# Kernel tuning notes

Measured on AMD Instinct MI355X. Metric: run time of the kernel, lower is better.

Reference implementation:

```python
import jax, jax.numpy as jnp
import numpy as np

B, T, E, H = 32, 577, 1024, 16
D = E // H  # head_dim = 64

def setup_inputs() -> dict:
    key = jax.random.key(0)
    ks = jax.random.split(key, 5)
    s = 1.0 / np.sqrt(E)
    return {
        "x": jax.random.normal(ks[0], (B, T, E), dtype=jnp.float32),
        "Wq": jax.random.normal(ks[1], (E, E), dtype=jnp.float32) * s,
        "bq": jnp.zeros((E,), dtype=jnp.float32),
        "Wk": jax.random.normal(ks[2], (E, E), dtype=jnp.float32) * s,
        "bk": jnp.zeros((E,), dtype=jnp.float32),
        "Wv": jax.random.normal(ks[3], (E, E), dtype=jnp.float32) * s,
        "bv": jnp.zeros((E,), dtype=jnp.float32),
        "Wo": jax.random.normal(ks[4], (E, E), dtype=jnp.float32) * s,
        "bo": jnp.zeros((E,), dtype=jnp.float32),
    }

def reference(x, Wq, bq, Wk, bk, Wv, bv, Wo, bo):
    # Linear projections (torch Linear: x @ W.T + b; here W stored as [in,out])
    q = (x @ Wq + bq).reshape(B, T, H, D).transpose(0, 2, 1, 3)  # [B,H,T,D]
    k = (x @ Wk + bk).reshape(B, T, H, D).transpose(0, 2, 1, 3)
    v = (x @ Wv + bv).reshape(B, T, H, D).transpose(0, 2, 1, 3)
    scores = jnp.einsum('bhqd,bhkd->bhqk', q, k) / jnp.sqrt(jnp.float32(D))
    att = jax.nn.softmax(scores, axis=-1)  # dropout is identity in eval
    out = jnp.einsum('bhqk,bhkd->bhqd', att, v)
    out = out.transpose(0, 2, 1, 3).reshape(B, T, E)
    return out @ Wo + bo
```

## Files before the change

kernel.cpp:

```cpp
#include <hip/hip_runtime.h>
#include <cmath>

#define BDIM 32
#define TDIM 577
#define TPAD 640
#define EDIM 1024
#define HDIM 16
#define DDIM 64
#define MDIM (BDIM * TDIM)
#define MTILES 145
#define MPAD (MTILES * 128)

typedef unsigned short u16;
typedef __bf16 bf16x8 __attribute__((ext_vector_type(8)));
typedef float f32x4 __attribute__((ext_vector_type(4)));
typedef u16 u16x8 __attribute__((ext_vector_type(8)));

__device__ __forceinline__ u16 f2bf(float f) {
    unsigned int u = __float_as_uint(f);
    u = (u + 0x7FFFu + ((u >> 16) & 1u)) >> 16;
    return (u16)u;
}

__device__ __forceinline__ void gload_lds16(const void* g, void* l) {
    __builtin_amdgcn_global_load_lds(
        (const __attribute__((address_space(1))) unsigned int*)g,
        (__attribute__((address_space(3))) unsigned int*)l, 16, 0, 0);
}

__global__ __launch_bounds__(256) void cast_x(const float* __restrict__ x,
                                              u16* __restrict__ o, int nelem)
{
    int i = (blockIdx.x * 256 + threadIdx.x) * 8;
    if (i >= nelem) return;
    float4 a = *(const float4*)(x + i);
    float4 b = *(const float4*)(x + i + 4);
    u16x8 r;
    r[0] = f2bf(a.x); r[1] = f2bf(a.y); r[2] = f2bf(a.z); r[3] = f2bf(a.w);
    r[4] = f2bf(b.x); r[5] = f2bf(b.y); r[6] = f2bf(b.z); r[7] = f2bf(b.w);
    *(u16x8*)(o + i) = r;
}

__global__ __launch_bounds__(256) void cast_wt(
    const float* __restrict__ W0, const float* __restrict__ W1,
    const float* __restrict__ W2, const float* __restrict__ W3,
    u16* __restrict__ T0, u16* __restrict__ T1,
    u16* __restrict__ T2, u16* __restrict__ T3)
{
    __shared__ float tile[32][33];
    const int z = blockIdx.z;
    const float* __restrict__ W = (z == 0) ? W0 : (z == 1) ? W1 : (z == 2) ? W2 : W3;
    u16* __restrict__ T = (z == 0) ? T0 : (z == 1) ? T1 : (z == 2) ? T2 : T3;
    const int bn = blockIdx.x * 32;
    const int bk = blockIdx.y * 32;
    const int tx = threadIdx.x & 31, ty = threadIdx.x >> 5;
#pragma unroll
    for (int p = 0; p < 4; ++p) {
        int k = bk + p * 8 + ty;
        tile[p * 8 + ty][tx] = W[(size_t)k * EDIM + bn + tx];
    }
    __syncthreads();
#pragma unroll
    for (int p = 0; p < 4; ++p) {
        int n = bn + p * 8 + ty;
        T[(size_t)n * EDIM + bk + tx] = f2bf(tile[tx][p * 8 + ty]);
    }
}

__global__ __launch_bounds__(256, 4) void gemm_bf16(
    const u16* __restrict__ A,
    const u16* __restrict__ W0, const u16* __restrict__ W1, const u16* __restrict__ W2,
    const float* __restrict__ b0, const float* __restrict__ b1, const float* __restrict__ b2,
    void* __restrict__ o0, void* __restrict__ o1, void* __restrict__ o2,
    int mode)
{
    __shared__ u16 As[128 * 64];
    __shared__ u16 Bs[128 * 64];

    const int z = blockIdx.z;
    const u16* __restrict__ Wt     = (z == 0) ? W0 : ((z == 1) ? W1 : W2);
    const float* __restrict__ bias = (z == 0) ? b0 : ((z == 1) ? b1 : b2);
    void* __restrict__ dst         = (z == 0) ? o0 : ((z == 1) ? o1 : o2);

    const int tid = threadIdx.x;
    const int wave = tid >> 6;
    const int lane = tid & 63;
    const int mlane = lane & 15;
    const int quad = lane >> 4;
    const int wm = wave >> 1;
    const int wn = wave & 1;
    const int m0 = blockIdx.y * 128;
    const int n0 = blockIdx.x * 128;

    f32x4 acc[4][4];
#pragma unroll
    for (int i = 0; i < 4; ++i)
#pragma unroll
        for (int j = 0; j < 4; ++j) acc[i][j] = (f32x4)(0.f);

    for (int k0 = 0; k0 < EDIM; k0 += 64) {
#pragma unroll
        for (int r = 0; r < 4; ++r) {
            int c = r * 256 + tid;
            int p = c >> 9, row = (c >> 2) & 127, j4 = c & 3;
            int koff = k0 + p * 32 + j4 * 8;
            gload_lds16(A + (size_t)(m0 + row) * EDIM + koff,
                        &As[(r * 256 + wave * 64) * 8]);
            gload_lds16(Wt + (size_t)(n0 + row) * EDIM + koff,
                        &Bs[(r * 256 + wave * 64) * 8]);
        }
        __syncthreads();

#pragma unroll
        for (int ks = 0; ks < 2; ++ks) {
            bf16x8 af[4], bfr[4];
#pragma unroll
            for (int t = 0; t < 4; ++t) {
                af[t]  = *(const bf16x8*)&As[ks * 4096 + (wm * 64 + t * 16 + mlane) * 32 + quad * 8];
                bfr[t] = *(const bf16x8*)&Bs[ks * 4096 + (wn * 64 + t * 16 + mlane) * 32 + quad * 8];
            }
#pragma unroll
            for (int i = 0; i < 4; ++i)
#pragma unroll
                for (int j = 0; j < 4; ++j)
                    acc[i][j] = __builtin_amdgcn_mfma_f32_16x16x32_bf16(af[i], bfr[j], acc[i][j], 0, 0, 0);
        }
        __syncthreads();
    }

#pragma unroll
    for (int j = 0; j < 4; ++j) {
        int n = n0 + wn * 64 + j * 16 + mlane;
        float bv = bias[n];
        if (mode == 1) {
            float* df = (float*)dst;
#pragma unroll
            for (int i = 0; i < 4; ++i) {
                int mb = m0 + wm * 64 + i * 16 + quad * 4;
#pragma unroll
                for (int r = 0; r < 4; ++r) {
                    int gm = mb + r;
                    if (gm < MDIM) df[(size_t)gm * EDIM + n] = acc[i][j][r] + bv;
                }
            }
        } else {
            u16* db = (u16*)dst;
            int h = n >> 6, d = n & 63;
#pragma unroll
            for (int i = 0; i < 4; ++i) {
                int mb = m0 + wm * 64 + i * 16 + quad * 4;
#pragma unroll
                for (int r = 0; r < 4; ++r) {
                    int gm = mb + r;
                    if (gm < MDIM) {
                        int b = gm / TDIM, t = gm - b * TDIM;
                        u16 val = f2bf(acc[i][j][r] + bv);
                        if (z == 2)
                            db[((size_t)(b * HDIM + h) * DDIM + d) * TPAD + t] = val;
                        else
                            db[((size_t)(b * HDIM + h) * TPAD + t) * DDIM + d] = val;
                    }
                }
            }
        }
    }
}

__global__ __launch_bounds__(256) void attn_mfma(
    const u16* __restrict__ qg, const u16* __restrict__ kg,
    const u16* __restrict__ vtg, u16* __restrict__ outg)
{
    __shared__ u16 Qs[4096];
    __shared__ u16 Ks[4096];
    __shared__ u16 Vts[4096];
    __shared__ u16 Ps[4608];

    const int tid = threadIdx.x;
    const int wave = tid >> 6;
    const int lane = tid & 63;
    const int ml = lane & 15;
    const int quad = lane >> 4;
    const int h = blockIdx.y, b = blockIdx.z;
    const int q0 = blockIdx.x * 64;
    const u16* qb = qg + ((size_t)b * HDIM + h) * TPAD * DDIM;
    const u16* kb = kg + ((size_t)b * HDIM + h) * TPAD * DDIM;
    const u16* vb = vtg + ((size_t)b * HDIM + h) * DDIM * TPAD;

#pragma unroll
    for (int r = 0; r < 2; ++r) {
        int c = r * 256 + tid;
        int row = (c >> 2) & 63, kc = c >> 8, d8 = c & 3;
        gload_lds16(qb + (size_t)(q0 + row) * DDIM + kc * 32 + d8 * 8,
                    &Qs[(r * 256 + wave * 64) * 8]);
    }
    __syncthreads();

    bf16x8 aq0 = *(const bf16x8*)&Qs[(wave * 16 + ml) * 32 + quad * 8];
    bf16x8 aq1 = *(const bf16x8*)&Qs[2048 + (wave * 16 + ml) * 32 + quad * 8];

    f32x4 oacc[4];
#pragma unroll
    for (int dt = 0; dt < 4; ++dt) oacc[dt] = (f32x4)(0.f);
    float m_i[4], l_i[4];
#pragma unroll
    for (int r = 0; r < 4; ++r) { m_i[r] = -INFINITY; l_i[r] = 0.f; }

    for (int kv0 = 0; kv0 < TDIM; kv0 += 64) {
        __syncthreads();
#pragma unroll
        for (int r = 0; r < 2; ++r) {
            int c = r * 256 + tid;
            int row = (c >> 2) & 63, kc = c >> 8, d8 = c & 3;
            gload_lds16(kb + (size_t)(kv0 + row) * DDIM + kc * 32 + d8 * 8,
                        &Ks[(r * 256 + wave * 64) * 8]);
            gload_lds16(vb + (size_t)row * TPAD + kv0 + kc * 32 + d8 * 8,
                        &Vts[(r * 256 + wave * 64) * 8]);
        }
        __syncthreads();

        f32x4 sacc[4];
#pragma unroll
        for (int jt = 0; jt < 4; ++jt) {
            bf16x8 bk0 = *(const bf16x8*)&Ks[(jt * 16 + ml) * 32 + quad * 8];
            bf16x8 bk1 = *(const bf16x8*)&Ks[2048 + (jt * 16 + ml) * 32 + quad * 8];
            f32x4 sa = (f32x4)(0.f);
            sa = __builtin_amdgcn_mfma_f32_16x16x32_bf16(aq0, bk0, sa, 0, 0, 0);
            sa = __builtin_amdgcn_mfma_f32_16x16x32_bf16(aq1, bk1, sa, 0, 0, 0);
            sacc[jt] = sa;
        }

        float p[4][4];
#pragma unroll
        for (int r = 0; r < 4; ++r) {
            float cm = -INFINITY;
#pragma unroll
            for (int jt = 0; jt < 4; ++jt) {
                bool valid = (kv0 + jt * 16 + ml) < TDIM;
                float sv = valid ? sacc[jt][r] * 0.125f : -INFINITY;
                p[jt][r] = sv;
                cm = fmaxf(cm, sv);
            }
            cm = fmaxf(cm, __shfl_xor(cm, 1, 64));
            cm = fmaxf(cm, __shfl_xor(cm, 2, 64));
            cm = fmaxf(cm, __shfl_xor(cm, 4, 64));
            cm = fmaxf(cm, __shfl_xor(cm, 8, 64));
            float mn = fmaxf(m_i[r], cm);
            float alpha = __expf(m_i[r] - mn);
            float rs = 0.f;
#pragma unroll
            for (int jt = 0; jt < 4; ++jt) {
                float e = __expf(p[jt][r] - mn);
                p[jt][r] = e;
                rs += e;
            }
            rs += __shfl_xor(rs, 1, 64);
            rs += __shfl_xor(rs, 2, 64);
            rs += __shfl_xor(rs, 4, 64);
            rs += __shfl_xor(rs, 8, 64);
            l_i[r] = l_i[r] * alpha + rs;
            m_i[r] = mn;
#pragma unroll
            for (int dt = 0; dt < 4; ++dt) oacc[dt][r] *= alpha;
        }

#pragma unroll
        for (int jt = 0; jt < 4; ++jt)
#pragma unroll
            for (int r = 0; r < 4; ++r)
                Ps[wave * 1152 + (jt >> 1) * 576 + (quad * 4 + r) * 36 + (jt & 1) * 16 + ml]
                    = f2bf(p[jt][r]);
        __syncthreads();

        bf16x8 pf0 = *(const bf16x8*)&Ps[wave * 1152 + ml * 36 + quad * 8];
        bf16x8 pf1 = *(const bf16x8*)&Ps[wave * 1152 + 576 + ml * 36 + quad * 8];

#pragma unroll
        for (int dt = 0; dt < 4; ++dt) {
            bf16x8 bv0 = *(const bf16x8*)&Vts[(dt * 16 + ml) * 32 + quad * 8];
            bf16x8 bv1 = *(const bf16x8*)&Vts[2048 + (dt * 16 + ml) * 32 + quad * 8];
            oacc[dt] = __builtin_amdgcn_mfma_f32_16x16x32_bf16(pf0, bv0, oacc[dt], 0, 0, 0);
            oacc[dt] = __builtin_amdgcn_mfma_f32_16x16x32_bf16(pf1, bv1, oacc[dt], 0, 0, 0);
        }
    }

#pragma unroll
    for (int r = 0; r < 4; ++r) {
        int t = q0 + wave * 16 + quad * 4 + r;
        if (t >= TDIM) continue;
        float inv = 1.f / l_i[r];
        size_t rowoff = ((size_t)b * TDIM + t) * EDIM + h * DDIM;
#pragma unroll
        for (int dt = 0; dt < 4; ++dt)
            outg[rowoff + dt * 16 + ml] = f2bf(oacc[dt][r] * inv);
    }
}

extern "C" void kernel_launch(void* const* d_in, const int* in_sizes, int n_in,
                              void* d_out, int out_size, void* d_ws, size_t ws_size,
                              hipStream_t stream)
{
    const float* x  = (const float*)d_in[0];
    const float* Wq = (const float*)d_in[1];
    const float* bq = (const float*)d_in[2];
    const float* Wk = (const float*)d_in[3];
    const float* bk = (const float*)d_in[4];
    const float* Wv = (const float*)d_in[5];
    const float* bv = (const float*)d_in[6];
    const float* Wo = (const float*)d_in[7];
    const float* bo = (const float*)d_in[8];
    float* out = (float*)d_out;

    const size_t hsz = (size_t)BDIM * HDIM * TPAD * DDIM;
    u16* qb  = (u16*)d_ws;
    u16* kb  = qb + hsz;
    u16* vtb = kb + hsz;
    u16* xb  = vtb + hsz;
    u16* abb = xb;
    u16* wtq = xb + (size_t)MPAD * EDIM;
    u16* wtk = wtq + (size_t)EDIM * EDIM;
    u16* wtv = wtk + (size_t)EDIM * EDIM;
    u16* wto = wtv + (size_t)EDIM * EDIM;

    cast_x<<<(MDIM * EDIM / 8 + 255) / 256, 256, 0, stream>>>(x, xb, MDIM * EDIM);
    cast_wt<<<dim3(32, 32, 4), 256, 0, stream>>>(Wq, Wk, Wv, Wo, wtq, wtk, wtv, wto);

    gemm_bf16<<<dim3(EDIM / 128, MTILES, 3), 256, 0, stream>>>(
        xb, wtq, wtk, wtv, bq, bk, bv, (void*)qb, (void*)kb, (void*)vtb, 0);

    attn_mfma<<<dim3(TPAD / 64, HDIM, BDIM), 256, 0, stream>>>(qb, kb, vtb, abb);

    gemm_bf16<<<dim3(EDIM / 128, MTILES, 1), 256, 0, stream>>>(
        abb, wto, wto, wto, bo, bo, bo, (void*)out, (void*)out, (void*)out, 1);
}
```

Measured before the change: 612.2 us.

## Loop Q/K/V projections inside one block, fold softmax scale into Q, split GEMM kernels

The QKV projection kernel now runs the three projections in sequence inside each block instead of using a z grid dimension. Consecutive passes reuse the same A tile rows, which may then hit in cache, while the launch has a third as many blocks, each doing three times the work. The 1/sqrt(D) scale is folded into the Q epilogue before bf16 rounding, and the attention kernel skips masking on full key tiles. The output projection becomes its own specialised kernel without the mode branch. Fewer blocks give less parallelism and a longer tail, and scaling Q before rounding slightly changes numerics.

```diff
diff --git a/kernel.cpp b/kernel.cpp
--- a/kernel.cpp
+++ b/kernel.cpp
@@ -67,20 +67,14 @@
     }
 }
 
-__global__ __launch_bounds__(256, 4) void gemm_bf16(
-    const u16* __restrict__ A,
-    const u16* __restrict__ W0, const u16* __restrict__ W1, const u16* __restrict__ W2,
-    const float* __restrict__ b0, const float* __restrict__ b1, const float* __restrict__ b2,
-    void* __restrict__ o0, void* __restrict__ o1, void* __restrict__ o2,
-    int mode)
+__global__ __launch_bounds__(256, 4) void gemm_qkv(
+    const u16* __restrict__ A, const u16* __restrict__ Wt,
+    const float* __restrict__ bq, const float* __restrict__ bk,
+    const float* __restrict__ bv,
+    u16* __restrict__ qo, u16* __restrict__ ko, u16* __restrict__ vto)
 {
     __shared__ u16 As[128 * 64];
     __shared__ u16 Bs[128 * 64];
-
-    const int z = blockIdx.z;
-    const u16* __restrict__ Wt     = (z == 0) ? W0 : ((z == 1) ? W1 : W2);
-    const float* __restrict__ bias = (z == 0) ? b0 : ((z == 1) ? b1 : b2);
-    void* __restrict__ dst         = (z == 0) ? o0 : ((z == 1) ? o1 : o2);
 
     const int tid = threadIdx.x;
     const int wave = tid >> 6;
@@ -92,6 +86,91 @@
     const int m0 = blockIdx.y * 128;
     const int n0 = blockIdx.x * 128;
 
+    for (int z = 0; z < 3; ++z) {
+        const u16* __restrict__ W = Wt + (size_t)z * EDIM * EDIM;
+        const float* __restrict__ bias = (z == 0) ? bq : ((z == 1) ? bk : bv);
+        u16* __restrict__ dst = (z == 0) ? qo : ((z == 1) ? ko : vto);
+
+        f32x4 acc[4][4];
+#pragma unroll
+        for (int i = 0; i < 4; ++i)
+#pragma unroll
+            for (int j = 0; j < 4; ++j) acc[i][j] = (f32x4)(0.f);
+
+        for (int k0 = 0; k0 < EDIM; k0 += 64) {
+#pragma unroll
+            for (int r = 0; r < 4; ++r) {
+                int c = r * 256 + tid;
+                int p = c >> 9, row = (c >> 2) & 127, j4 = c & 3;
+                int koff = k0 + p * 32 + j4 * 8;
+                gload_lds16(A + (size_t)(m0 + row) * EDIM + koff,
+                            &As[(r * 256 + wave * 64) * 8]);
+                gload_lds16(W + (size_t)(n0 + row) * EDIM + koff,
+                            &Bs[(r * 256 + wave * 64) * 8]);
+            }
+            __syncthreads();
+
+#pragma unroll
+            for (int ks = 0; ks < 2; ++ks) {
+                bf16x8 af[4], bfr[4];
+#pragma unroll
+                for (int t = 0; t < 4; ++t) {
+                    af[t]  = *(const bf16x8*)&As[ks * 4096 + (wm * 64 + t * 16 + mlane) * 32 + quad * 8];
+                    bfr[t] = *(const bf16x8*)&Bs[ks * 4096 + (wn * 64 + t * 16 + mlane) * 32 + quad * 8];
+                }
+#pragma unroll
+                for (int i = 0; i < 4; ++i)
+#pragma unroll
+                    for (int j = 0; j < 4; ++j)
+                        acc[i][j] = __builtin_amdgcn_mfma_f32_16x16x32_bf16(af[i], bfr[j], acc[i][j], 0, 0, 0);
+            }
+            __syncthreads();
+        }
+
+#pragma unroll
+        for (int j = 0; j < 4; ++j) {
+            int n = n0 + wn * 64 + j * 16 + mlane;
+            float bvv = bias[n];
+            int h = n >> 6, d = n & 63;
+#pragma unroll
+            for (int i = 0; i < 4; ++i) {
+                int mb = m0 + wm * 64 + i * 16 + quad * 4;
+#pragma unroll
+                for (int r = 0; r < 4; ++r) {
+                    int gm = mb + r;
+                    if (gm < MDIM) {
+                        int b = gm / TDIM, t = gm - b * TDIM;
+                        float val = acc[i][j][r] + bvv;
+                        if (z == 0) val *= 0.125f;
+                        u16 vb16 = f2bf(val);
+                        if (z == 2)
+                            dst[((size_t)(b * HDIM + h) * DDIM + d) * TPAD + t] = vb16;
+                        else
+                            dst[((size_t)(b * HDIM + h) * TPAD + t) * DDIM + d] = vb16;
+                    }
+                }
+            }
+        }
+    }
+}
+
+__global__ __launch_bounds__(256, 4) void gemm_out(
+    const u16* __restrict__ A, const u16* __restrict__ Wt,
+    const float* __restrict__ bias, float* __restrict__ dst)
+{
+    __shared__ u16 As[128 * 64];
+    __shared__ u16 Bs[128 * 64];
+
+    const int tid = threadIdx.x;
+    const int wave = tid >> 6;
+    const int lane = tid & 63;
+    const int mlane = lane & 15;
+    const int quad = lane >> 4;
+    const int wm = wave >> 1;
+    const int wn = wave & 1;
+    const int m0 = blockIdx.y * 128;
+    const int n0 = blockIdx.x * 128;
+
     f32x4 acc[4][4];
 #pragma unroll
     for (int i = 0; i < 4; ++i)
@@ -131,36 +210,14 @@
 #pragma unroll
     for (int j = 0; j < 4; ++j) {
         int n = n0 + wn * 64 + j * 16 + mlane;
-        float bv = bias[n];
-        if (mode == 1) {
-            float* df = (float*)dst;
-#pragma unroll
-            for (int i = 0; i < 4; ++i) {
-                int mb = m0 + wm * 64 + i * 16 + quad * 4;
-#pragma unroll
-                for (int r = 0; r < 4; ++r) {
-                    int gm = mb + r;
-                    if (gm < MDIM) df[(size_t)gm * EDIM + n] = acc[i][j][r] + bv;
-                }
-            }
-        } else {
-            u16* db = (u16*)dst;
-            int h = n >> 6, d = n & 63;
-#pragma unroll
-            for (int i = 0; i < 4; ++i) {
-                int mb = m0 + wm * 64 + i * 16 + quad * 4;
-#pragma unroll
-                for (int r = 0; r < 4; ++r) {
-                    int gm = mb + r;
-                    if (gm < MDIM) {
-                        int b = gm / TDIM, t = gm - b * TDIM;
-                        u16 val = f2bf(acc[i][j][r] + bv);
-                        if (z == 2)
-                            db[((size_t)(b * HDIM + h) * DDIM + d) * TPAD + t] = val;
-                        else
-                            db[((size_t)(b * HDIM + h) * TPAD + t) * DDIM + d] = val;
-                    }
-                }
+        float bvv = bias[n];
+#pragma unroll
+        for (int i = 0; i < 4; ++i) {
+            int mb = m0 + wm * 64 + i * 16 + quad * 4;
+#pragma unroll
+            for (int r = 0; r < 4; ++r) {
+                int gm = mb + r;
+                if (gm < MDIM) dst[(size_t)gm * EDIM + n] = acc[i][j][r] + bvv;
             }
         }
     }
@@ -230,15 +287,23 @@
         }
 
         float p[4][4];
+        const bool full = (kv0 + 64 <= TDIM);
 #pragma unroll
         for (int r = 0; r < 4; ++r) {
-            float cm = -INFINITY;
-#pragma unroll
-            for (int jt = 0; jt < 4; ++jt) {
-                bool valid = (kv0 + jt * 16 + ml) < TDIM;
-                float sv = valid ? sacc[jt][r] * 0.125f : -INFINITY;
-                p[jt][r] = sv;
-                cm = fmaxf(cm, sv);
+            float cm;
+            if (full) {
+#pragma unroll
+                for (int jt = 0; jt < 4; ++jt) p[jt][r] = sacc[jt][r];
+                cm = fmaxf(fmaxf(p[0][r], p[1][r]), fmaxf(p[2][r], p[3][r]));
+            } else {
+                cm = -INFINITY;
+#pragma unroll
+                for (int jt = 0; jt < 4; ++jt) {
+                    bool valid = (kv0 + jt * 16 + ml) < TDIM;
+                    float sv = valid ? sacc[jt][r] : -INFINITY;
+                    p[jt][r] = sv;
+                    cm = fmaxf(cm, sv);
+                }
             }
             cm = fmaxf(cm, __shfl_xor(cm, 1, 64));
             cm = fmaxf(cm, __shfl_xor(cm, 2, 64));
@@ -324,11 +389,10 @@
     cast_x<<<(MDIM * EDIM / 8 + 255) / 256, 256, 0, stream>>>(x, xb, MDIM * EDIM);
     cast_wt<<<dim3(32, 32, 4), 256, 0, stream>>>(Wq, Wk, Wv, Wo, wtq, wtk, wtv, wto);
 
-    gemm_bf16<<<dim3(EDIM / 128, MTILES, 3), 256, 0, stream>>>(
-        xb, wtq, wtk, wtv, bq, bk, bv, (void*)qb, (void*)kb, (void*)vtb, 0);
+    gemm_qkv<<<dim3(EDIM / 128, MTILES), 256, 0, stream>>>(
+        xb, wtq, bq, bk, bv, qb, kb, vtb);
 
     attn_mfma<<<dim3(TPAD / 64, HDIM, BDIM), 256, 0, stream>>>(qb, kb, vtb, abb);
 
-    gemm_bf16<<<dim3(EDIM / 128, MTILES, 1), 256, 0, stream>>>(
-        abb, wto, wto, wto, bo, bo, bo, (void*)out, (void*)out, (void*)out, 1);
-}
+    gemm_out<<<dim3(EDIM / 128, MTILES), 256, 0, stream>>>(abb, wto, bo, out);
+}
```

After: 810.5 us. 32.4% more time.
